# Performance work log

Measured on AMD Instinct MI355X. Metric: run time of the kernel, lower is better.

Reference implementation:

```python
import jax, jax.numpy as jnp
import numpy as np

HOP = 32  # stride from init_kwargs


def setup_inputs() -> dict:
    key = jax.random.key(0)
    kc, kv = jax.random.split(key)
    B, N, K, L = 8, 512, 32768, 64
    c = jax.random.normal(kc, (B, N, K), dtype=jnp.float32)
    V = jax.random.normal(kv, (L, N), dtype=jnp.float32) * 0.01
    return {"c": c, "V": V}


def reference(c, V):
    # c: [B, N, K], V: [L, N]
    B, N, K = c.shape
    L = V.shape[0]
    T_out = (K - 1) * HOP + L
    # all per-frame projections in one batched GEMM: [B, K, L]
    frames = jnp.einsum('ln,bnk->bkl', V, c)
    # overlap-add: frame k writes to samples [k*HOP, k*HOP+L)
    idx = (jnp.arange(K)[:, None] * HOP + jnp.arange(L)[None, :]).reshape(-1)  # [K*L]
    y = jnp.zeros((B, T_out), dtype=c.dtype).at[:, idx].add(frames.reshape(B, K * L))
    return y[:, None, :]  # [B, 1, T_out]
```

## Files before the change

kernel.cpp:

```cpp
#include <hip/hip_runtime.h>
#include <hip/hip_bf16.h>

#define HOP 32
#define NB 8
#define NDIM 512
#define KDIM 32768
#define LDIM 64
#define TOUT ((KDIM - 1) * HOP + LDIM)
#define QTILE 64
#define CT_ROWS 72
#define NSPLIT 128
#define CT_STRIDE 136

typedef __bf16 bf16x8 __attribute__((ext_vector_type(8)));
typedef float floatx4 __attribute__((ext_vector_type(4)));

__device__ __forceinline__ unsigned short f2bf(float f) {
    unsigned int u = __float_as_uint(f);
    u += 0x7FFFu + ((u >> 16) & 1u);
    return (unsigned short)(u >> 16);
}

__global__ void convert_v_kernel(const float* __restrict__ vf,
                                 unsigned short* __restrict__ vb) {
    int i = (blockIdx.x * 256 + threadIdx.x) * 4;
    float4 v = *reinterpret_cast<const float4*>(vf + i);
    ushort4 o;
    o.x = f2bf(v.x); o.y = f2bf(v.y); o.z = f2bf(v.z); o.w = f2bf(v.w);
    *reinterpret_cast<ushort4*>(vb + i) = o;
}

__global__ __launch_bounds__(256, 4) void decoder_kernel(
        const float* __restrict__ cg,
        const unsigned short* __restrict__ vb,
        float* __restrict__ outg)
{
    __shared__ __align__(16) unsigned short ct[2][CT_ROWS * CT_STRIDE];

    const int tid  = threadIdx.x;
    const int tile = blockIdx.x;
    const int b    = blockIdx.y;
    const int q0   = tile * QTILE;
    const int lane = tid & 63;

    const long cbase = (long)b * NDIM * KDIM;
    const bool fastA = (q0 + QTILE <= KDIM);
    const bool fastB = (q0 >= 8);

    const int w   = tid >> 6;
    const int l15 = lane & 15;
    const int g   = lane >> 4;
    const int jlo = w * 16 + l15;

    floatx4 acc0 = {0.f, 0.f, 0.f, 0.f};
    floatx4 acc1 = {0.f, 0.f, 0.f, 0.f};

    auto stage = [&](int n0, int s) {
        #pragma unroll
        for (int it = 0; it < 8; ++it) {
            int id = it * 256 + tid;
            int n  = id >> 4;
            int cc = id & 15;
            int colbase = q0 + cc * 4;
            float4 v;
            if (fastA) {
                v = *reinterpret_cast<const float4*>(cg + cbase + (long)(n0 + n) * KDIM + colbase);
            } else {
                float* ve = reinterpret_cast<float*>(&v);
                #pragma unroll
                for (int e = 0; e < 4; ++e) {
                    int col = colbase + e;
                    ve[e] = (col < KDIM) ? cg[cbase + (long)(n0 + n) * KDIM + col] : 0.f;
                }
            }
            unsigned short sr[4];
            sr[0] = f2bf(v.x); sr[1] = f2bf(v.y); sr[2] = f2bf(v.z); sr[3] = f2bf(v.w);
            #pragma unroll
            for (int i = 0; i < 4; ++i) {
                int e = (lane + i) & 3;
                ct[s][(8 + cc * 4 + e) * CT_STRIDE + n] = sr[e];
            }
        }
        {
            int n  = tid >> 1;
            int cc = tid & 1;
            int colbase = q0 - 8 + cc * 4;
            float4 v;
            if (fastB) {
                v = *reinterpret_cast<const float4*>(cg + cbase + (long)(n0 + n) * KDIM + colbase);
            } else {
                float* ve = reinterpret_cast<float*>(&v);
                #pragma unroll
                for (int e = 0; e < 4; ++e) {
                    int col = colbase + e;
                    ve[e] = (col >= 0) ? cg[cbase + (long)(n0 + n) * KDIM + col] : 0.f;
                }
            }
            unsigned short sr[4];
            sr[0] = f2bf(v.x); sr[1] = f2bf(v.y); sr[2] = f2bf(v.z); sr[3] = f2bf(v.w);
            #pragma unroll
            for (int i = 0; i < 4; ++i) {
                int e = (lane + i) & 3;
                ct[s][(cc * 4 + e) * CT_STRIDE + n] = sr[e];
            }
        }
    };

    auto mma = [&](int n0, int s) {
        #pragma unroll
        for (int ks = 0; ks < 8; ++ks) {
            const int hi   = (ks >= 4);
            const int ncol = (ks & 3) * 32 + g * 8;
            const unsigned short* bp = &ct[s][(jlo + (hi ? 7 : 8)) * CT_STRIDE + ncol];
            bf16x8 bfrag = *reinterpret_cast<const bf16x8*>(bp);
            const int vrow0 = l15 + (hi ? 32 : 0);
            bf16x8 a0 = *reinterpret_cast<const bf16x8*>(vb + vrow0 * NDIM + n0 + ncol);
            bf16x8 a1 = *reinterpret_cast<const bf16x8*>(vb + (vrow0 + 16) * NDIM + n0 + ncol);
            acc0 = __builtin_amdgcn_mfma_f32_16x16x32_bf16(a0, bfrag, acc0, 0, 0, 0);
            acc1 = __builtin_amdgcn_mfma_f32_16x16x32_bf16(a1, bfrag, acc1, 0, 0, 0);
        }
    };

    stage(0, 0);
    __syncthreads();
    #pragma unroll
    for (int p = 0; p < 4; ++p) {
        if (p < 3) stage((p + 1) * NSPLIT, (p + 1) & 1);
        mma(p * NSPLIT, p & 1);
        __syncthreads();
    }

    const int q = q0 + w * 16 + l15;
    if (q <= KDIM) {
        long tb = (long)b * TOUT + (long)q * HOP + g * 4;
        *reinterpret_cast<floatx4*>(outg + tb)      = acc0;
        *reinterpret_cast<floatx4*>(outg + tb + 16) = acc1;
    }
}

extern "C" void kernel_launch(void* const* d_in, const int* in_sizes, int n_in,
                              void* d_out, int out_size, void* d_ws, size_t ws_size,
                              hipStream_t stream) {
    const float* c  = (const float*)d_in[0];
    const float* V  = (const float*)d_in[1];
    float* out      = (float*)d_out;
    unsigned short* vb = (unsigned short*)d_ws;

    convert_v_kernel<<<dim3(32), dim3(256), 0, stream>>>(V, vb);
    dim3 grid(KDIM / QTILE + 1, NB);
    decoder_kernel<<<grid, dim3(256, 1, 1), 0, stream>>>(c, vb, out);
}
```

Measured before the change: 795.3 us.

## Shrink halo, vectorize LDS staging writes, and remap tiles per XCD

Each thread now loads four consecutive c rows per column group, so it can pack the transposed bf16 values into one 8-byte LDS store instead of four scalar 2-byte stores. The halo shrinks from 8 to 4 columns because only one previous frame's column is needed, which cuts the extra halo loads. Block indices are also remapped so each XCD handles a contiguous range of tiles, aiming at better L2 locality for the overlapping halo reads. The new mapping adds index arithmetic, and the per-thread row grouping changes the global access pattern.

```diff
diff --git a/kernel.cpp b/kernel.cpp
--- a/kernel.cpp
+++ b/kernel.cpp
@@ -8,7 +8,8 @@
 #define LDIM 64
 #define TOUT ((KDIM - 1) * HOP + LDIM)
 #define QTILE 64
-#define CT_ROWS 72
+#define HALO 4
+#define CT_ROWS 68
 #define NSPLIT 128
 #define CT_STRIDE 136
 
@@ -38,14 +39,18 @@
     __shared__ __align__(16) unsigned short ct[2][CT_ROWS * CT_STRIDE];
 
     const int tid  = threadIdx.x;
-    const int tile = blockIdx.x;
     const int b    = blockIdx.y;
+    const int lane = tid & 63;
+
+    const int nwg  = gridDim.x;
+    const int qd   = nwg >> 3, r = nwg & 7;
+    const int xcd  = blockIdx.x & 7, idx = blockIdx.x >> 3;
+    const int tile = (xcd < r ? xcd * (qd + 1) : r * (qd + 1) + (xcd - r) * qd) + idx;
     const int q0   = tile * QTILE;
-    const int lane = tid & 63;
 
     const long cbase = (long)b * NDIM * KDIM;
     const bool fastA = (q0 + QTILE <= KDIM);
-    const bool fastB = (q0 >= 8);
+    const bool fastB = (q0 >= HALO);
 
     const int w   = tid >> 6;
     const int l15 = lane & 15;
@@ -55,39 +60,53 @@
     floatx4 acc0 = {0.f, 0.f, 0.f, 0.f};
     floatx4 acc1 = {0.f, 0.f, 0.f, 0.f};
 
-    auto stage = [&](int n0, int s) {
+    auto stage = [&](int n0, int sb) {
         #pragma unroll
-        for (int it = 0; it < 8; ++it) {
+        for (int it = 0; it < 2; ++it) {
             int id = it * 256 + tid;
-            int n  = id >> 4;
+            int nq = id >> 4;
             int cc = id & 15;
             int colbase = q0 + cc * 4;
-            float4 v;
+            float4 v[4];
             if (fastA) {
-                v = *reinterpret_cast<const float4*>(cg + cbase + (long)(n0 + n) * KDIM + colbase);
+                #pragma unroll
+                for (int rr = 0; rr < 4; ++rr)
+                    v[rr] = *reinterpret_cast<const float4*>(
+                        cg + cbase + (long)(n0 + 4 * nq + rr) * KDIM + colbase);
             } else {
-                float* ve = reinterpret_cast<float*>(&v);
                 #pragma unroll
-                for (int e = 0; e < 4; ++e) {
-                    int col = colbase + e;
-                    ve[e] = (col < KDIM) ? cg[cbase + (long)(n0 + n) * KDIM + col] : 0.f;
+                for (int rr = 0; rr < 4; ++rr) {
+                    float* ve = reinterpret_cast<float*>(&v[rr]);
+                    #pragma unroll
+                    for (int e = 0; e < 4; ++e) {
+                        int col = colbase + e;
+                        ve[e] = (col < KDIM)
+                              ? cg[cbase + (long)(n0 + 4 * nq + rr) * KDIM + col] : 0.f;
+                    }
                 }
             }
-            unsigned short sr[4];
-            sr[0] = f2bf(v.x); sr[1] = f2bf(v.y); sr[2] = f2bf(v.z); sr[3] = f2bf(v.w);
+            unsigned short s4[4][4];
+            #pragma unroll
+            for (int rr = 0; rr < 4; ++rr) {
+                s4[rr][0] = f2bf(v[rr].x); s4[rr][1] = f2bf(v[rr].y);
+                s4[rr][2] = f2bf(v[rr].z); s4[rr][3] = f2bf(v[rr].w);
+            }
             #pragma unroll
             for (int i = 0; i < 4; ++i) {
-                int e = (lane + i) & 3;
-                ct[s][(8 + cc * 4 + e) * CT_STRIDE + n] = sr[e];
+                int ee = (lane + i) & 3;
+                ushort4 w4;
+                w4.x = s4[0][ee]; w4.y = s4[1][ee]; w4.z = s4[2][ee]; w4.w = s4[3][ee];
+                *reinterpret_cast<ushort4*>(
+                    &ct[sb][(HALO + cc * 4 + ee) * CT_STRIDE + 4 * nq]) = w4;
             }
         }
-        {
-            int n  = tid >> 1;
-            int cc = tid & 1;
-            int colbase = q0 - 8 + cc * 4;
+        if (tid < 128) {
+            int n = tid;
+            int colbase = q0 - HALO;
             float4 v;
             if (fastB) {
-                v = *reinterpret_cast<const float4*>(cg + cbase + (long)(n0 + n) * KDIM + colbase);
+                v = *reinterpret_cast<const float4*>(
+                    cg + cbase + (long)(n0 + n) * KDIM + colbase);
             } else {
                 float* ve = reinterpret_cast<float*>(&v);
                 #pragma unroll
@@ -100,18 +119,19 @@
             sr[0] = f2bf(v.x); sr[1] = f2bf(v.y); sr[2] = f2bf(v.z); sr[3] = f2bf(v.w);
             #pragma unroll
             for (int i = 0; i < 4; ++i) {
-                int e = (lane + i) & 3;
-                ct[s][(cc * 4 + e) * CT_STRIDE + n] = sr[e];
+                int ee = (lane + i) & 3;
+                ct[sb][ee * CT_STRIDE + n] = sr[ee];
             }
         }
     };
 
-    auto mma = [&](int n0, int s) {
+    auto mma = [&](int n0, int sb) {
         #pragma unroll
         for (int ks = 0; ks < 8; ++ks) {
             const int hi   = (ks >= 4);
             const int ncol = (ks & 3) * 32 + g * 8;
-            const unsigned short* bp = &ct[s][(jlo + (hi ? 7 : 8)) * CT_STRIDE + ncol];
+            const unsigned short* bp =
+                &ct[sb][(jlo + (hi ? HALO - 1 : HALO)) * CT_STRIDE + ncol];
             bf16x8 bfrag = *reinterpret_cast<const bf16x8*>(bp);
             const int vrow0 = l15 + (hi ? 32 : 0);
             bf16x8 a0 = *reinterpret_cast<const bf16x8*>(vb + vrow0 * NDIM + n0 + ncol);
```

Result: faster. 762.2 us (-4.2%).
